# Kernel tuning notes

Hardware: AMD Instinct MI355X
Metric: run time of the kernel (lower is better)

Reference implementation:

```python
import jax, jax.numpy as jnp
import numpy as np


def _lstm(x, Wih, Whh, bih, bhh):
    # x: [T,B,E] -> outputs [T,B,H]; torch gate order i,f,g,o
    B = x.shape[1]
    H = Whh.shape[1]
    bias = bih + bhh
    def step(carry, xt):
        h, c = carry
        g = xt @ Wih.T + h @ Whh.T + bias  # [B,4H]
        i, f, gg, o = jnp.split(g, 4, axis=-1)
        c = jax.nn.sigmoid(f) * c + jax.nn.sigmoid(i) * jnp.tanh(gg)
        h = jax.nn.sigmoid(o) * jnp.tanh(c)
        return (h, c), h
    init = (jnp.zeros((B, H), x.dtype), jnp.zeros((B, H), x.dtype))
    _, hs = jax.lax.scan(step, init, x)
    return hs


def setup_inputs():
    key = jax.random.key(0)
    ks = jax.random.split(key, 16)
    B, T, V, NT, E, H = 128, 512, 50000, 24, 128, 256
    Hd = H // 2  # per-direction hidden
    s = 0.08
    x = jax.random.randint(ks[0], (B, T), 0, V)
    tags = jax.random.randint(ks[1], (B, T), 0, NT)
    lengths = jax.random.randint(ks[2], (B,), T // 2, T + 1)
    mask = jnp.arange(T)[None, :] < lengths[:, None]  # [B,T] bool, position 0 always valid
    emb = (jax.random.normal(ks[3], (V, E)) * s).at[0].set(0.0)  # padding_idx=0 row zeroed
    Wih_f = jax.random.normal(ks[4], (4 * Hd, E)) * s
    Whh_f = jax.random.normal(ks[5], (4 * Hd, Hd)) * s
    bih_f = jax.random.normal(ks[6], (4 * Hd,)) * s
    bhh_f = jax.random.normal(ks[7], (4 * Hd,)) * s
    Wih_b = jax.random.normal(ks[8], (4 * Hd, E)) * s
    Whh_b = jax.random.normal(ks[9], (4 * Hd, Hd)) * s
    bih_b = jax.random.normal(ks[10], (4 * Hd,)) * s
    bhh_b = jax.random.normal(ks[11], (4 * Hd,)) * s
    W_out = jax.random.normal(ks[12], (NT, H)) * s
    b_out = jnp.zeros((NT,))
    transitions = jax.random.normal(ks[13], (NT, NT))
    start_trans = jax.random.normal(ks[14], (NT,))
    end_trans = jax.random.normal(ks[15], (NT,))
    return {"x": x, "tags": tags, "mask": mask, "emb": emb,
            "Wih_f": Wih_f, "Whh_f": Whh_f, "bih_f": bih_f, "bhh_f": bhh_f,
            "Wih_b": Wih_b, "Whh_b": Whh_b, "bih_b": bih_b, "bhh_b": bhh_b,
            "W_out": W_out, "b_out": b_out, "transitions": transitions,
            "start_trans": start_trans, "end_trans": end_trans}


def reference(x, tags, mask, emb, Wih_f, Whh_f, bih_f, bhh_f,
              Wih_b, Whh_b, bih_b, bhh_b, W_out, b_out,
              transitions, start_trans, end_trans):
    # --- emissions (dropout is identity in eval) ---
    xe = emb[x]                       # [B,T,E]
    xt = xe.transpose(1, 0, 2)        # [T,B,E]
    hf = _lstm(xt, Wih_f, Whh_f, bih_f, bhh_f)               # [T,B,Hd]
    hb = _lstm(xt[::-1], Wih_b, Whh_b, bih_b, bhh_b)[::-1]   # [T,B,Hd]
    h = jnp.concatenate([hf, hb], axis=-1).transpose(1, 0, 2)  # [B,T,H]
    emissions = h @ W_out.T + b_out   # [B,T,NT]

    # --- CRF forward algorithm (logZ) via scan over time ---
    score0 = start_trans + emissions[:, 0]  # [B,NT]
    em_rest = emissions[:, 1:].transpose(1, 0, 2)  # [T-1,B,NT]
    m_rest = mask[:, 1:].T                        # [T-1,B]
    def fwd_step(score, inp):
        em_t, m_t = inp
        ns = jax.nn.logsumexp(score[:, :, None] + transitions[None] + em_t[:, None, :], axis=1)
        return jnp.where(m_t[:, None], ns, score), None
    score, _ = jax.lax.scan(fwd_step, score0, (em_rest, m_rest))
    logZ = jax.nn.logsumexp(score + end_trans, axis=1)  # [B]

    # --- gold path score, fully vectorized ---
    mf = mask.astype(emissions.dtype)
    emit = jnp.take_along_axis(emissions, tags[:, :, None], axis=2)[:, :, 0]  # [B,T]
    trans = transitions[tags[:, :-1], tags[:, 1:]]                            # [B,T-1]
    gold = start_trans[tags[:, 0]] + emit[:, 0] + jnp.sum((trans + emit[:, 1:]) * mf[:, 1:], axis=1)
    last_idx = mask.sum(axis=1) - 1
    last_tags = jnp.take_along_axis(tags, last_idx[:, None], axis=1)[:, 0]
    gold = gold + end_trans[last_tags]

    return jnp.mean(logZ - gold)
```

## Files before the change

kernel.cpp:

```cpp
#include <hip/hip_runtime.h>
#include <hip/hip_bf16.h>

typedef unsigned short u16;
typedef unsigned int   u32;
typedef _Float16 half2_t __attribute__((ext_vector_type(2)));
typedef short    bf16x8 __attribute__((ext_vector_type(8)));
typedef float    f32x4  __attribute__((ext_vector_type(4)));
typedef u32      u32x4v __attribute__((ext_vector_type(4)));

#define TT   512

__device__ __forceinline__ float sigf(float x)  { return 1.0f / (1.0f + __expf(-x)); }
__device__ __forceinline__ float tanhf_(float x){ return 1.0f - 2.0f / (__expf(2.0f * x) + 1.0f); }

__device__ __forceinline__ u16 f2bf(float x) {
  __hip_bfloat16 h = __float2bfloat16(x);
  return *reinterpret_cast<u16*>(&h);
}
__device__ __forceinline__ float bf2f(u16 u) { return __uint_as_float(((u32)u) << 16); }
__device__ __forceinline__ u32 pk2(float a, float b) {
  return (u32)f2bf(a) | ((u32)f2bf(b) << 16);
}
__device__ __forceinline__ u16 f2h(float x) {
  _Float16 h = (_Float16)x;
  union { _Float16 f; u16 u; } c; c.f = h; return c.u;
}
__device__ __forceinline__ half2_t u2h2(u32 v) {
  union { u32 u; half2_t h; } c; c.u = v; return c.h;
}

__global__ __launch_bounds__(256) void prep_k(
    const float* __restrict__ Wih_f, const float* __restrict__ Wih_b,
    const float* __restrict__ Whh_f, const float* __restrict__ Whh_b,
    const float* __restrict__ bih_f, const float* __restrict__ bhh_f,
    const float* __restrict__ bih_b, const float* __restrict__ bhh_b,
    const float* __restrict__ W_out,
    u16* __restrict__ Wb, u16* __restrict__ Whhb, float* __restrict__ bias,
    u32* __restrict__ Wout16)
{
  int i = blockIdx.x * 256 + threadIdx.x;
  {
    int n = i >> 7, k = i & 127;
    int d = n >> 9, rem = n & 511, uu = rem >> 2, g = rem & 3;
    const float* W = d ? Wih_b : Wih_f;
    Wb[i] = f2bf(W[(g * 128 + uu) * 128 + k]);
  }
  {
    int d = i >> 16, rem = i & 65535, n = rem >> 7, k = rem & 127;
    const float* W = d ? Whh_b : Whh_f;
    Whhb[i] = f2bf(W[n * 128 + k]);
  }
  if (i < 1024) {
    int d = i >> 9, rem = i & 511, uu = rem >> 2, g = rem & 3;
    int src = g * 128 + uu;
    bias[i] = d ? (bih_b[src] + bhh_b[src]) : (bih_f[src] + bhh_f[src]);
  }
  if (i < 3072) {
    Wout16[i] = (u32)f2h(W_out[2 * i]) | ((u32)f2h(W_out[2 * i + 1]) << 16);
  }
}

__global__ __launch_bounds__(256, 2) void gates_mfma_k(
    const int* __restrict__ x, const float* __restrict__ emb,
    const u16* __restrict__ Wb, const float* __restrict__ bias,
    u16* __restrict__ Gout)
{
  const int tid = threadIdx.x;
  const int wid = tid >> 6, l = tid & 63;
  const int wm = wid >> 1, wn = wid & 1;
  const int M0 = blockIdx.y * 128, N0 = blockIdx.x * 128;
  const int lr = l & 15, lk = l >> 4;

  int tok[4];
#pragma unroll
  for (int mi = 0; mi < 4; ++mi)
    tok[mi] = x[M0 + wm * 64 + mi * 16 + lr];

  f32x4 acc[4][4];
#pragma unroll
  for (int i = 0; i < 4; ++i)
#pragma unroll
    for (int j = 0; j < 4; ++j) acc[i][j] = (f32x4){0.f, 0.f, 0.f, 0.f};

#pragma unroll
  for (int ks = 0; ks < 4; ++ks) {
    bf16x8 a[4], b[4];
#pragma unroll
    for (int mi = 0; mi < 4; ++mi) {
      const float* ep = emb + (size_t)tok[mi] * 128 + ks * 32 + lk * 8;
      float4 v0 = *(const float4*)ep;
      float4 v1 = *(const float4*)(ep + 4);
      union { u32 u[4]; bf16x8 v; } cvt;
      cvt.u[0] = pk2(v0.x, v0.y); cvt.u[1] = pk2(v0.z, v0.w);
      cvt.u[2] = pk2(v1.x, v1.y); cvt.u[3] = pk2(v1.z, v1.w);
      a[mi] = cvt.v;
    }
#pragma unroll
    for (int ni = 0; ni < 4; ++ni)
      b[ni] = *(const bf16x8*)&Wb[(size_t)(N0 + wn * 64 + ni * 16 + lr) * 128 + ks * 32 + lk * 8];
#pragma unroll
    for (int mi = 0; mi < 4; ++mi)
#pragma unroll
      for (int ni = 0; ni < 4; ++ni)
        acc[mi][ni] = __builtin_amdgcn_mfma_f32_16x16x32_bf16(a[mi], b[ni], acc[mi][ni], 0, 0, 0);
  }

  float bcol[4];
#pragma unroll
  for (int ni = 0; ni < 4; ++ni) bcol[ni] = bias[N0 + wn * 64 + ni * 16 + lr];

  __shared__ u16 cs[128][136];
#pragma unroll
  for (int mi = 0; mi < 4; ++mi)
#pragma unroll
    for (int ni = 0; ni < 4; ++ni) {
      int col = wn * 64 + ni * 16 + lr;
#pragma unroll
      for (int r = 0; r < 4; ++r) {
        int row = wm * 64 + mi * 16 + lk * 4 + r;
        cs[row][col] = f2bf(acc[mi][ni][r] + bcol[ni]);
      }
    }
  __syncthreads();
  {
    int row = tid >> 1, c0 = (tid & 1) * 64;
    u16* dst = &Gout[(size_t)(M0 + row) * 1024 + N0 + c0];
#pragma unroll
    for (int q = 0; q < 8; ++q)
      *(uint4*)&dst[q * 8] = *(const uint4*)&cs[row][c0 + q * 8];
  }
}

__global__ __launch_bounds__(512, 1) void lstm_mfma_k(
    const u16* __restrict__ G, const u16* __restrict__ Whhb,
    u16* __restrict__ Hout)
{
  const int bid = blockIdx.x;
  const int dir = bid >> 7;
  const int b   = bid & 127;
  const int tid = threadIdx.x;
  const int w = tid >> 6, l = tid & 63;
  const int lr = l & 15, lk = l >> 4;
  const int u = 16 * w + lr;

  const u16* wbase = Whhb + ((size_t)dir << 16);
  bf16x8 B[4][4];
#pragma unroll
  for (int g = 0; g < 4; ++g)
#pragma unroll
    for (int ks = 0; ks < 4; ++ks)
      B[g][ks] = *(const bf16x8*)&wbase[(size_t)(g * 128 + u) * 128 + ks * 32 + lk * 8];

  __shared__ u16 hl[2][16][136];

  for (int i = tid; i < 2 * 16 * 136; i += 512) ((u16*)hl)[i] = 0;

  float cc = 0.f;
  const int ts = dir ? -1 : 1;
  const int t0 = dir ? (TT - 1) : 0;
  const long gstride = (long)ts * 1024;
  const long hstride = (long)ts * 256;

  const u16* gptr = G + ((size_t)b * 512 + t0) * 1024 + dir * 512 + u * 4;
  u16*       hptr = Hout + ((size_t)b * 512 + t0) * 256 + dir * 128 + u;

  ushort4 qcur = *(const ushort4*)gptr;
  gptr += gstride;
  u16 hprev = 0;
  __syncthreads();

  for (int s = 0; s < TT; ++s) {
    const int cb = s & 1, wb = cb ^ 1;

    ushort4 qnext = qcur;
    if (s + 1 < TT) { qnext = *(const ushort4*)gptr; gptr += gstride; }
    if (s > 0)      { if (lk == 0) *hptr = hprev; hptr += hstride; }

    bf16x8 A[4];
#pragma unroll
    for (int ks = 0; ks < 4; ++ks)
      A[ks] = *(const bf16x8*)&hl[cb][lr][ks * 32 + lk * 8];
    f32x4 acc[4];
#pragma unroll
    for (int g = 0; g < 4; ++g) acc[g] = (f32x4){0.f, 0.f, 0.f, 0.f};
#pragma unroll
    for (int ks = 0; ks < 4; ++ks)
#pragma unroll
      for (int g = 0; g < 4; ++g)
        acc[g] = __builtin_amdgcn_mfma_f32_16x16x32_bf16(A[ks], B[g][ks], acc[g], 0, 0, 0);

    if (lk == 0) {
      float gi = acc[0][0] + bf2f(qcur.x);
      float gf = acc[1][0] + bf2f(qcur.y);
      float gg = acc[2][0] + bf2f(qcur.z);
      float go = acc[3][0] + bf2f(qcur.w);
      float iv = sigf(gi), fv = sigf(gf), gv = tanhf_(gg), ov = sigf(go);
      cc = fv * cc + iv * gv;
      float hv = ov * tanhf_(cc);
      hl[wb][0][u] = f2bf(hv);
      hprev = f2h(hv);
    }
    __syncthreads();
    qcur = qnext;
  }
  if (lk == 0) *hptr = hprev;
}

__global__ __launch_bounds__(256) void emis_k(
    const u16* __restrict__ Hb, const u32* __restrict__ Wout16,
    const float* __restrict__ b_out, float* __restrict__ em)
{
  __shared__ __align__(16) u32 wl2[24 * 128];
  __shared__ float bo[24];
  const int tid = threadIdx.x;
  for (int i = tid; i < 3072; i += 256) wl2[i] = Wout16[i];
  if (tid < 24) bo[tid] = b_out[tid];
  __syncthreads();

  const int m = blockIdx.x * 256 + tid;
  float acc[24];
#pragma unroll
  for (int tg = 0; tg < 24; ++tg) acc[tg] = bo[tg];

  const u32* h2 = (const u32*)(Hb + (size_t)m * 256);
  for (int ck = 0; ck < 16; ++ck) {
    uint4 hv = *(const uint4*)(h2 + ck * 4);
#pragma unroll
    for (int tg = 0; tg < 24; ++tg) {
      u32x4v wv = *(const u32x4v*)&wl2[tg * 128 + ck * 4];
      float a = acc[tg];
      a = __builtin_amdgcn_fdot2(u2h2(hv.x), u2h2(wv.x), a, false);
      a = __builtin_amdgcn_fdot2(u2h2(hv.y), u2h2(wv.y), a, false);
      a = __builtin_amdgcn_fdot2(u2h2(hv.z), u2h2(wv.z), a, false);
      a = __builtin_amdgcn_fdot2(u2h2(hv.w), u2h2(wv.w), a, false);
      acc[tg] = a;
    }
  }
#pragma unroll
  for (int t6 = 0; t6 < 6; ++t6) {
    float4 o;
    o.x = acc[t6*4+0]; o.y = acc[t6*4+1]; o.z = acc[t6*4+2]; o.w = acc[t6*4+3];
    *(float4*)&em[(size_t)m * 24 + t6 * 4] = o;
  }
}

__device__ __forceinline__ int get_mask(const void* mp, int idx, bool byte_mode) {
  return byte_mode ? (int)((const unsigned char*)mp)[idx] : ((const int*)mp)[idx];
}

__global__ __launch_bounds__(64) void crf_k(
    const float* __restrict__ em, const int* __restrict__ tags,
    const void* __restrict__ maskp, const float* __restrict__ trans,
    const float* __restrict__ start_tr, const float* __restrict__ end_tr,
    float* __restrict__ out)
{
  const int b = blockIdx.x;
  const int tid = threadIdx.x;
  const bool byte_mode = (*(const u32*)maskp != 1u);
  const bool act = (tid < 48);
  const int j  = (tid < 24) ? tid : (act ? tid - 24 : 0);
  const int i0 = (tid < 24) ? 0 : 12;
  const int partner = (tid < 24) ? tid + 24 : tid - 24;

  int cnt = 0;
  for (int t = tid; t < TT; t += 64) cnt += get_mask(maskp, b * TT + t, byte_mode);
#pragma unroll
  for (int off = 32; off > 0; off >>= 1) cnt += __shfl_down(cnt, off);
  cnt = __shfl(cnt, 0);

  float Texp[12];
  if (act) {
#pragma unroll
    for (int k = 0; k < 12; ++k) Texp[k] = __expf(trans[(i0 + k) * 24 + j]);
  } else {
#pragma unroll
    for (int k = 0; k < 12; ++k) Texp[k] = 0.f;
  }

  float sc0 = act ? (start_tr[j] + em[(size_t)(b * TT) * 24 + j]) : -1e30f;
  float m = sc0;
#pragma unroll
  for (int off = 32; off > 0; off >>= 1) m = fmaxf(m, __shfl_xor(m, off));
  float P = act ? __expf(sc0 - m) : 0.f;
  float logC = m;

  float em_next = 0.f;
  if (act && cnt > 1) em_next = em[(size_t)(b * TT + 1) * 24 + j];
  float eem_next = __expf(em_next);

  for (int t = 1; t < cnt; ++t) {
    float eem = eem_next;
    if (act && t + 1 < cnt) em_next = em[(size_t)(b * TT + t + 1) * 24 + j];

    float s0 = 0.f, s1 = 0.f, s2 = 0.f;
#pragma unroll
    for (int k = 0; k < 4; ++k)  s0 += __shfl(P, i0 + k)     * Texp[k];
#pragma unroll
    for (int k = 4; k < 8; ++k)  s1 += __shfl(P, i0 + k)     * Texp[k];
#pragma unroll
    for (int k = 8; k < 12; ++k) s2 += __shfl(P, i0 + k)     * Texp[k];
    float sh = (s0 + s1) + s2;
    float so = __shfl(sh, partner);
    float tot = sh + so;
    eem_next = __expf(em_next);
    P = act ? (eem * tot) : 0.f;

    if ((t & 7) == 0) {
      float mm = P;
#pragma unroll
      for (int off = 32; off > 0; off >>= 1) mm = fmaxf(mm, __shfl_xor(mm, off));
      P = P / mm;
      logC += __logf(mm);
    }
  }

  float z = (tid < 24) ? P * __expf(end_tr[tid]) : 0.f;
#pragma unroll
  for (int off = 32; off > 0; off >>= 1) z += __shfl_xor(z, off);
  float lzv = logC + __logf(z);

  float part = 0.f;
  for (int t = tid; t < TT; t += 64) {
    if (t >= 1 && t < cnt) {
      int tp = tags[b * TT + t - 1], tc = tags[b * TT + t];
      part += trans[tp * 24 + tc] + em[((size_t)(b * TT + t)) * 24 + tc];
    }
  }
#pragma unroll
  for (int off = 32; off > 0; off >>= 1) part += __shfl_down(part, off);
  if (tid == 0) {
    int t0g = tags[b * TT];
    float gold = start_tr[t0g] + em[(size_t)(b * TT) * 24 + t0g] + part;
    gold += end_tr[tags[b * TT + cnt - 1]];
    atomicAdd(out, (lzv - gold) * (1.0f / 128.0f));
  }
}

extern "C" void kernel_launch(void* const* d_in, const int* in_sizes, int n_in,
                              void* d_out, int out_size, void* d_ws, size_t ws_size,
                              hipStream_t stream) {
  const int*   x     = (const int*)d_in[0];
  const int*   tags  = (const int*)d_in[1];
  const void*  mask  = d_in[2];
  const float* emb   = (const float*)d_in[3];
  const float* Wih_f = (const float*)d_in[4];
  const float* Whh_f = (const float*)d_in[5];
  const float* bih_f = (const float*)d_in[6];
  const float* bhh_f = (const float*)d_in[7];
  const float* Wih_b = (const float*)d_in[8];
  const float* Whh_b = (const float*)d_in[9];
  const float* bih_b = (const float*)d_in[10];
  const float* bhh_b = (const float*)d_in[11];
  const float* W_out = (const float*)d_in[12];
  const float* b_out = (const float*)d_in[13];
  const float* trans = (const float*)d_in[14];
  const float* st_tr = (const float*)d_in[15];
  const float* en_tr = (const float*)d_in[16];

  u16*   Gb     = (u16*)d_ws;
  u16*   Hb     = Gb + (size_t)65536 * 1024;
  float* em     = (float*)(Hb + (size_t)65536 * 256);
  float* bias   = em + (size_t)65536 * 24;
  u16*   Wb     = (u16*)(bias + 1024);
  u16*   Whhb   = Wb + 131072;
  u32*   Wout16 = (u32*)(Whhb + 131072);

  prep_k<<<512, 256, 0, stream>>>(Wih_f, Wih_b, Whh_f, Whh_b,
                                  bih_f, bhh_f, bih_b, bhh_b, W_out,
                                  Wb, Whhb, bias, Wout16);
  gates_mfma_k<<<dim3(8, 512), 256, 0, stream>>>(x, emb, Wb, bias, Gb);
  lstm_mfma_k<<<256, 512, 0, stream>>>(Gb, Whhb, Hb);
  emis_k<<<256, 256, 0, stream>>>(Hb, Wout16, b_out, em);
  (void)hipMemsetAsync(d_out, 0, sizeof(float), stream);
  crf_k<<<128, 64, 0, stream>>>(em, tags, mask, trans, st_tr, en_tr, (float*)d_out);
}
```

Measured before the change: 626.2 us.

## Move emissions to bf16 MFMA, repack CRF batches per block, swap gate grid order

Replaces the per-thread fdot2 emission kernel with a bf16 MFMA GEMM that reads W_out padded to 32 columns, and the LSTM now stores h as bf16 instead of fp16. The gates kernel grid is transposed so adjacent blocks walk along M rather than N, and the LSTM's shared h buffer row pitch is widened, presumably to change the LDS bank pattern. The CRF kernel packs 8 sequences per 512-thread block instead of one per 64-thread block. These are several unrelated tweaks; the MFMA emission kernel recomputes global B loads per wave, and moving h to bf16 lowers its precision.

```diff
diff --git a/kernel.cpp b/kernel.cpp
--- a/kernel.cpp
+++ b/kernel.cpp
@@ -24,9 +24,6 @@
 __device__ __forceinline__ u16 f2h(float x) {
   _Float16 h = (_Float16)x;
   union { _Float16 f; u16 u; } c; c.f = h; return c.u;
-}
-__device__ __forceinline__ half2_t u2h2(u32 v) {
-  union { u32 u; half2_t h; } c; c.u = v; return c.h;
 }
 
 __global__ __launch_bounds__(256) void prep_k(
@@ -36,7 +33,7 @@
     const float* __restrict__ bih_b, const float* __restrict__ bhh_b,
     const float* __restrict__ W_out,
     u16* __restrict__ Wb, u16* __restrict__ Whhb, float* __restrict__ bias,
-    u32* __restrict__ Wout16)
+    u16* __restrict__ Woutb)
 {
   int i = blockIdx.x * 256 + threadIdx.x;
   {
@@ -55,8 +52,9 @@
     int src = g * 128 + uu;
     bias[i] = d ? (bih_b[src] + bhh_b[src]) : (bih_f[src] + bhh_f[src]);
   }
-  if (i < 3072) {
-    Wout16[i] = (u32)f2h(W_out[2 * i]) | ((u32)f2h(W_out[2 * i + 1]) << 16);
+  if (i < 8192) {
+    int n = i >> 8, k = i & 255;
+    Woutb[i] = (n < 24) ? f2bf(W_out[n * 256 + k]) : (u16)0;
   }
 }
 
@@ -68,7 +66,7 @@
   const int tid = threadIdx.x;
   const int wid = tid >> 6, l = tid & 63;
   const int wm = wid >> 1, wn = wid & 1;
-  const int M0 = blockIdx.y * 128, N0 = blockIdx.x * 128;
+  const int M0 = blockIdx.x * 128, N0 = blockIdx.y * 128;
   const int lr = l & 15, lk = l >> 4;
 
   int tok[4];
@@ -151,9 +149,9 @@
     for (int ks = 0; ks < 4; ++ks)
       B[g][ks] = *(const bf16x8*)&wbase[(size_t)(g * 128 + u) * 128 + ks * 32 + lk * 8];
 
-  __shared__ u16 hl[2][16][136];
-
-  for (int i = tid; i < 2 * 16 * 136; i += 512) ((u16*)hl)[i] = 0;
+  __shared__ u16 hl[2][16][168];
+
+  for (int i = tid; i < 2 * 16 * 168; i += 512) ((u16*)hl)[i] = 0;
 
   float cc = 0.f;
   const int ts = dir ? -1 : 1;
@@ -197,8 +195,9 @@
       float iv = sigf(gi), fv = sigf(gf), gv = tanhf_(gg), ov = sigf(go);
       cc = fv * cc + iv * gv;
       float hv = ov * tanhf_(cc);
-      hl[wb][0][u] = f2bf(hv);
-      hprev = f2h(hv);
+      u16 hb = f2bf(hv);
+      hl[wb][0][u] = hb;
+      hprev = hb;
     }
     __syncthreads();
     qcur = qnext;
@@ -206,56 +205,65 @@
   if (lk == 0) *hptr = hprev;
 }
 
-__global__ __launch_bounds__(256) void emis_k(
-    const u16* __restrict__ Hb, const u32* __restrict__ Wout16,
+__global__ __launch_bounds__(256) void emis_mfma_k(
+    const u16* __restrict__ Hb, const u16* __restrict__ Woutb,
     const float* __restrict__ b_out, float* __restrict__ em)
 {
-  __shared__ __align__(16) u32 wl2[24 * 128];
-  __shared__ float bo[24];
   const int tid = threadIdx.x;
-  for (int i = tid; i < 3072; i += 256) wl2[i] = Wout16[i];
-  if (tid < 24) bo[tid] = b_out[tid];
-  __syncthreads();
-
-  const int m = blockIdx.x * 256 + tid;
-  float acc[24];
-#pragma unroll
-  for (int tg = 0; tg < 24; ++tg) acc[tg] = bo[tg];
-
-  const u32* h2 = (const u32*)(Hb + (size_t)m * 256);
-  for (int ck = 0; ck < 16; ++ck) {
-    uint4 hv = *(const uint4*)(h2 + ck * 4);
-#pragma unroll
-    for (int tg = 0; tg < 24; ++tg) {
-      u32x4v wv = *(const u32x4v*)&wl2[tg * 128 + ck * 4];
-      float a = acc[tg];
-      a = __builtin_amdgcn_fdot2(u2h2(hv.x), u2h2(wv.x), a, false);
-      a = __builtin_amdgcn_fdot2(u2h2(hv.y), u2h2(wv.y), a, false);
-      a = __builtin_amdgcn_fdot2(u2h2(hv.z), u2h2(wv.z), a, false);
-      a = __builtin_amdgcn_fdot2(u2h2(hv.w), u2h2(wv.w), a, false);
-      acc[tg] = a;
-    }
-  }
-#pragma unroll
-  for (int t6 = 0; t6 < 6; ++t6) {
-    float4 o;
-    o.x = acc[t6*4+0]; o.y = acc[t6*4+1]; o.z = acc[t6*4+2]; o.w = acc[t6*4+3];
-    *(float4*)&em[(size_t)m * 24 + t6 * 4] = o;
-  }
+  const int wid = tid >> 6, l = tid & 63;
+  const int lr = l & 15, lk = l >> 4;
+  const int m0 = blockIdx.x * 128 + wid * 32;
+
+  f32x4 acc[2][2];
+#pragma unroll
+  for (int i = 0; i < 2; ++i)
+#pragma unroll
+    for (int j = 0; j < 2; ++j) acc[i][j] = (f32x4){0.f, 0.f, 0.f, 0.f};
+
+#pragma unroll
+  for (int ks = 0; ks < 8; ++ks) {
+    bf16x8 a[2], b[2];
+#pragma unroll
+    for (int mi = 0; mi < 2; ++mi)
+      a[mi] = *(const bf16x8*)&Hb[(size_t)(m0 + mi * 16 + lr) * 256 + ks * 32 + lk * 8];
+#pragma unroll
+    for (int ni = 0; ni < 2; ++ni)
+      b[ni] = *(const bf16x8*)&Woutb[(size_t)(ni * 16 + lr) * 256 + ks * 32 + lk * 8];
+#pragma unroll
+    for (int mi = 0; mi < 2; ++mi)
+#pragma unroll
+      for (int ni = 0; ni < 2; ++ni)
+        acc[mi][ni] = __builtin_amdgcn_mfma_f32_16x16x32_bf16(a[mi], b[ni], acc[mi][ni], 0, 0, 0);
+  }
+
+#pragma unroll
+  for (int mi = 0; mi < 2; ++mi)
+#pragma unroll
+    for (int ni = 0; ni < 2; ++ni) {
+      int col = ni * 16 + lr;
+      if (col < 24) {
+        float bo = b_out[col];
+#pragma unroll
+        for (int r = 0; r < 4; ++r) {
+          int row = m0 + mi * 16 + lk * 4 + r;
+          em[(size_t)row * 24 + col] = acc[mi][ni][r] + bo;
+        }
+      }
+    }
 }
 
 __device__ __forceinline__ int get_mask(const void* mp, int idx, bool byte_mode) {
   return byte_mode ? (int)((const unsigned char*)mp)[idx] : ((const int*)mp)[idx];
 }
 
-__global__ __launch_bounds__(64) void crf_k(
+__global__ __launch_bounds__(512, 1) void crf_k(
     const float* __restrict__ em, const int* __restrict__ tags,
     const void* __restrict__ maskp, const float* __restrict__ trans,
     const float* __restrict__ start_tr, const float* __restrict__ end_tr,
     float* __restrict__ out)
 {
-  const int b = blockIdx.x;
-  const int tid = threadIdx.x;
+  const int b   = blockIdx.x * 8 + (threadIdx.x >> 6);
+  const int tid = threadIdx.x & 63;
   const bool byte_mode = (*(const u32*)maskp != 1u);
   const bool act = (tid < 48);
   const int j  = (tid < 24) ? tid : (act ? tid - 24 : 0);
@@ -363,14 +371,14 @@
   float* bias   = em + (size_t)65536 * 24;
   u16*   Wb     = (u16*)(bias + 1024);
   u16*   Whhb   = Wb + 131072;
-  u32*   Wout16 = (u32*)(Whhb + 131072);
+  u16*   Woutb  = Whhb + 131072;
 
   prep_k<<<512, 256, 0, stream>>>(Wih_f, Wih_b, Whh_f, Whh_b,
                                   bih_f, bhh_f, bih_b, bhh_b, W_out,
-                                  Wb, Whhb, bias, Wout16);
-  gates_mfma_k<<<dim3(8, 512), 256, 0, stream>>>(x, emb, Wb, bias, Gb);
+                                  Wb, Whhb, bias, Woutb);
+  gates_mfma_k<<<dim3(512, 8), 256, 0, stream>>>(x, emb, Wb, bias, Gb);
   lstm_mfma_k<<<256, 512, 0, stream>>>(Gb, Whhb, Hb);
-  emis_k<<<256, 256, 0, stream>>>(Hb, Wout16, b_out, em);
+  emis_mfma_k<<<512, 256, 0, stream>>>(Hb, Woutb, b_out, em);
   (void)hipMemsetAsync(d_out, 0, sizeof(float), stream);
-  crf_k<<<128, 64, 0, stream>>>(em, tags, mask, trans, st_tr, en_tr, (float*)d_out);
-}
+  crf_k<<<16, 512, 0, stream>>>(em, tags, mask, trans, st_tr, en_tr, (float*)d_out);
+}
```

New measurement: 654.4 us. 1.05x slower.
